# Kernel optimization log

Hardware: AMD Instinct MI355X
Metric: run time of the kernel (lower is better)

Reference implementation:

```python
import jax, jax.numpy as jnp
import numpy as np

BIAS_VALUE = -1e30


def apply_rope(inputs, positions, max_wavelength=10000):
    # inputs: [B, T, H, Dh]; positions: [B, T]
    head_dim = inputs.shape[-1]
    fraction = 2 * jnp.arange(0, head_dim // 2) / head_dim
    timescale = max_wavelength ** fraction
    sinusoid_inp = positions[..., jnp.newaxis] / timescale[jnp.newaxis, :]  # [B, T, Dh/2]
    sinusoid_inp = sinusoid_inp[..., jnp.newaxis, :]                        # [B, T, 1, Dh/2]
    sin = jnp.sin(sinusoid_inp)
    cos = jnp.cos(sinusoid_inp)
    first_half, second_half = jnp.split(inputs, 2, axis=-1)
    first_part = first_half * cos - second_half * sin
    second_part = second_half * cos + first_half * sin
    return jnp.concatenate([first_part, second_part], axis=-1).astype(inputs.dtype)


def rms_norm(x, scale):
    var = jnp.mean(jnp.square(x), axis=-1, keepdims=True)
    return x * jax.lax.rsqrt(var + 1e-6) * (1 + scale)


def setup_inputs() -> dict:
    key = jax.random.key(0)
    ks = jax.random.split(key, 12)
    B, T, D, H, Dh = 4, 2048, 512, 8, 64
    q = jax.random.normal(ks[0], (B, T, D), jnp.float32)
    kv = jax.random.normal(ks[1], (B, T, D), jnp.float32)
    mask = jnp.broadcast_to(jnp.tril(jnp.ones((T, T), bool))[None, None], (B, 1, T, T))
    pos = jnp.broadcast_to(jnp.arange(T, dtype=jnp.int32), (B, T))
    s = 0.02
    return {
        "q": q, "kv": kv, "mask": mask, "q_positions": pos, "kv_positions": pos,
        "wq": jax.random.normal(ks[2], (D, H * Dh), jnp.float32) * s,
        "bq": jnp.zeros((H * Dh,), jnp.float32),
        "wk": jax.random.normal(ks[3], (D, H * Dh), jnp.float32) * s,
        "bk": jnp.zeros((H * Dh,), jnp.float32),
        "wv": jax.random.normal(ks[4], (D, H * Dh), jnp.float32) * s,
        "bv": jnp.zeros((H * Dh,), jnp.float32),
        "scale_q": jax.random.normal(ks[5], (Dh,), jnp.float32) * s,
        "scale_k": jax.random.normal(ks[6], (Dh,), jnp.float32) * s,
        "wo": jax.random.normal(ks[7], (H * Dh, D), jnp.float32) * s,
        "bo": jnp.zeros((D,), jnp.float32),
    }


def reference(q, kv, mask, q_positions, kv_positions,
              wq, bq, wk, bk, wv, bv, scale_q, scale_k, wo, bo):
    B, T, D = q.shape
    H = 8
    Dh = wq.shape[1] // H
    qk_size = Dh

    def proj(x, w, b):
        y = x @ w + b
        return y.reshape(*x.shape[:-1], H, -1)  # [B, T, H, Dh]

    query_heads = rms_norm(proj(q, wq, bq), scale_q)
    key_heads = rms_norm(proj(kv, wk, bk), scale_k)
    value_heads = proj(kv, wv, bv)

    query_heads = apply_rope(query_heads, q_positions)
    key_heads = apply_rope(key_heads, kv_positions)

    attn_logits = jnp.einsum('bthd,bThd->bhtT', query_heads, key_heads)
    attn_logits = attn_logits / np.sqrt(qk_size).astype(q.dtype)
    attn_logits = jnp.where(mask, attn_logits, BIAS_VALUE)
    attn_weights = jax.nn.softmax(attn_logits, axis=-1)
    attn_weights = jnp.where(mask, attn_weights, 0)
    attn = jnp.einsum('bhtT,bThd->bthd', attn_weights, value_heads)
    attn = attn.reshape(B, T, -1)
    return attn @ wo + bo
```

## Files before the change

### kernel.cpp

```cpp
#include <hip/hip_runtime.h>
#include <hip/hip_bf16.h>
#include <cstdint>

#define B_ 4
#define T_ 2048
#define D_ 512
#define H_ 8

typedef __bf16 bf16x8 __attribute__((ext_vector_type(8)));
typedef __bf16 bf16x4 __attribute__((ext_vector_type(4)));
typedef float f32x4 __attribute__((ext_vector_type(4)));

#define QSCALE 0.18033688011112042f
#define MSHIFT 16.0f

__device__ inline void gload_lds16(const void* g, void* l) {
    __builtin_amdgcn_global_load_lds(
        (const __attribute__((address_space(1))) void*)g,
        (__attribute__((address_space(3))) void*)l, 16, 0, 0);
}

__global__ void transpose_w4_kernel(const float* __restrict__ wq, const float* __restrict__ wk,
                                    const float* __restrict__ wv, const float* __restrict__ wo,
                                    __bf16* __restrict__ wqkvT, __bf16* __restrict__ woT) {
    __shared__ float tile[32][33];
    int z = blockIdx.z;
    const float* in = (z == 0) ? wq : (z == 1) ? wk : (z == 2) ? wv : wo;
    __bf16* out = (z < 3) ? wqkvT + (size_t)z * D_ * D_ : woT;
    int tx = threadIdx.x & 31, ty = threadIdx.x >> 5;
    int r0 = blockIdx.y * 32, c0 = blockIdx.x * 32;
#pragma unroll
    for (int i = 0; i < 4; i++)
        tile[ty + i * 8][tx] = in[(size_t)(r0 + ty + i * 8) * D_ + c0 + tx];
    __syncthreads();
#pragma unroll
    for (int i = 0; i < 4; i++)
        out[(size_t)(c0 + ty + i * 8) * D_ + r0 + tx] = (__bf16)tile[tx][ty + i * 8];
}

__global__ void rope_table_kernel(float2* __restrict__ tab) {
    int i = blockIdx.x * 256 + threadIdx.x;
    int p = i >> 5, d2 = i & 31;
    float inv_ts = exp2f((float)d2 * (-13.28771237954945f / 32.0f));
    float ang = (float)p * inv_ts;
    float sv, cv;
    __sincosf(ang, &sv, &cv);
    tab[i] = make_float2(cv, sv);
}

template<int MODE>
__global__ __launch_bounds__(256, 2) void gemm_tile_kernel(
    const float* __restrict__ Aq32, const float* __restrict__ Akv32,
    const __bf16* __restrict__ Xbf,
    const __bf16* __restrict__ WT,
    const float* __restrict__ biasQ, const float* __restrict__ biasK,
    const float* __restrict__ biasV,
    float* __restrict__ outf, __bf16* __restrict__ qh, __bf16* __restrict__ kh,
    __bf16* __restrict__ vt,
    const float* __restrict__ scale_q, const float* __restrict__ scale_k,
    const int* __restrict__ qpos, const int* __restrict__ kpos,
    const float2* __restrict__ rtab, int M, int Ntot, int K) {
    __shared__ __bf16 Ab[2][128 * 32];
    __shared__ __bf16 Bb[2][128 * 32];

    const int tid = threadIdx.x;
    const int lane = tid & 63, widx = tid >> 6;
    const int lo = lane & 15, hi = lane >> 4;
    const int wm = widx >> 1, wn = widx & 1;

    const int nwg = gridDim.x;
    const int q8 = nwg >> 3;
    int bid = blockIdx.x;
    int swz = (bid & 7) * q8 + (bid >> 3);
    const int ntn = Ntot >> 7;
    const int m0 = (swz / ntn) << 7;
    const int nt = swz % ntn;
    const int n0g = nt << 7;
    const int seg = (MODE == 3) ? (nt >> 2) : 0;

    const int srow = tid >> 2;
    const int sslot = tid & 3;

    const float* Af32 = (MODE == 3) ? ((seg > 0) ? Akv32 : Aq32) : nullptr;

    f32x4 acc[4][4] = {};

    auto stageB = [&](int kc, int bufi) {
#pragma unroll
        for (int i = 0; i < 2; i++) {
            int row = i * 64 + srow;
            int cs = sslot ^ ((row >> 1) & 3);
            gload_lds16(WT + (size_t)(n0g + row) * K + kc + cs * 8,
                        &Bb[bufi][(i * 64 + widx * 16) * 32]);
        }
    };
    auto stageA_bf = [&](int kc, int bufi) {
#pragma unroll
        for (int i = 0; i < 2; i++) {
            int row = i * 64 + srow;
            int cs = sslot ^ ((row >> 1) & 3);
            gload_lds16(Xbf + (size_t)(m0 + row) * K + kc + cs * 8,
                        &Ab[bufi][(i * 64 + widx * 16) * 32]);
        }
    };
    auto loadA32 = [&](float4 (&r)[2][2], int kc) {
#pragma unroll
        for (int i = 0; i < 2; i++) {
            const float* src = Af32 + (size_t)(m0 + i * 64 + srow) * K + kc + sslot * 8;
            r[i][0] = *reinterpret_cast<const float4*>(src);
            r[i][1] = *reinterpret_cast<const float4*>(src + 4);
        }
    };
    auto writeA32 = [&](float4 (&r)[2][2], int bufi) {
#pragma unroll
        for (int i = 0; i < 2; i++) {
            int row = i * 64 + srow;
            bf16x8 v = { (__bf16)r[i][0].x, (__bf16)r[i][0].y,
                         (__bf16)r[i][0].z, (__bf16)r[i][0].w,
                         (__bf16)r[i][1].x, (__bf16)r[i][1].y,
                         (__bf16)r[i][1].z, (__bf16)r[i][1].w };
            *reinterpret_cast<bf16x8*>(
                &Ab[bufi][row * 32 + ((sslot ^ ((row >> 1) & 3)) << 3)]) = v;
        }
    };
    auto compute = [&](int bufi) {
        bf16x8 a[4], bvec[4];
#pragma unroll
        for (int mf = 0; mf < 4; mf++) {
            int R = wm * 64 + mf * 16 + lo;
            a[mf] = *reinterpret_cast<const bf16x8*>(&Ab[bufi][R * 32 + ((hi ^ ((R >> 1) & 3)) << 3)]);
        }
#pragma unroll
        for (int nf = 0; nf < 4; nf++) {
            int R = wn * 64 + nf * 16 + lo;
            bvec[nf] = *reinterpret_cast<const bf16x8*>(&Bb[bufi][R * 32 + ((hi ^ ((R >> 1) & 3)) << 3)]);
        }
#pragma unroll
        for (int mf = 0; mf < 4; mf++)
#pragma unroll
            for (int nf = 0; nf < 4; nf++)
                acc[mf][nf] = __builtin_amdgcn_mfma_f32_16x16x32_bf16(a[mf], bvec[nf], acc[mf][nf], 0, 0, 0);
    };

    const int nks = K >> 5;
    int cur = 0;

    if constexpr (MODE == 3) {
        float4 rA[2][2], rB[2][2];
        auto step3 = [&](int ks, float4 (&rUse)[2][2], float4 (&rLoad)[2][2]) {
            if (ks + 2 < nks) loadA32(rLoad, (ks + 2) << 5);
            if (ks + 1 < nks) stageB((ks + 1) << 5, cur ^ 1);
            compute(cur);
            if (ks + 1 < nks) writeA32(rUse, cur ^ 1);
            __syncthreads();
            cur ^= 1;
        };
        loadA32(rA, 0);
        stageB(0, 0);
        writeA32(rA, 0);
        loadA32(rA, 32);
        __syncthreads();
        for (int ks = 0; ks < nks; ks += 2) {
            step3(ks, rA, rB);
            step3(ks + 1, rB, rA);
        }
    } else {
        stageA_bf(0, 0); stageB(0, 0);
        __syncthreads();
        for (int ks = 0; ks < nks; ks++) {
            const int kc2 = (ks + 1) << 5;
            if (ks + 1 < nks) { stageA_bf(kc2, cur ^ 1); stageB(kc2, cur ^ 1); }
            compute(cur);
            __syncthreads();
            cur ^= 1;
        }
    }

    const int mrow0 = m0 + wm * 64;

    if (MODE == 0) {
        const int ncol0 = n0g + wn * 64;
        float bs[4];
#pragma unroll
        for (int nf = 0; nf < 4; nf++) bs[nf] = biasQ[ncol0 + nf * 16 + lo];
#pragma unroll
        for (int mf = 0; mf < 4; mf++)
#pragma unroll
            for (int nf = 0; nf < 4; nf++)
#pragma unroll
                for (int r = 0; r < 4; r++) {
                    int row = mrow0 + mf * 16 + hi * 4 + r;
                    outf[(size_t)row * Ntot + ncol0 + nf * 16 + lo] = acc[mf][nf][r] + bs[nf];
                }
    } else {
        const int ncol0 = ((nt & 3) << 7) + wn * 64;
        const int h = ncol0 >> 6;
        const float* bias = (seg == 0) ? biasQ : (seg == 1) ? biasK : biasV;
        float bs[4];
#pragma unroll
        for (int nf = 0; nf < 4; nf++) bs[nf] = bias[ncol0 + nf * 16 + lo];

        if (seg < 2) {
            const float* scale = seg ? scale_k : scale_q;
            const int* pos = seg ? kpos : qpos;
            __bf16* dst0 = seg ? kh : qh;
            const float qmul = seg ? 1.0f : QSCALE;
            float sc4[4];
#pragma unroll
            for (int nf = 0; nf < 4; nf++) sc4[nf] = (1.0f + scale[nf * 16 + lo]) * qmul;
#pragma unroll
            for (int mf = 0; mf < 4; mf++) {
#pragma unroll
                for (int r = 0; r < 4; r++) {
                    int row = mrow0 + mf * 16 + hi * 4 + r;
                    float y0 = acc[mf][0][r] + bs[0];
                    float y1 = acc[mf][1][r] + bs[1];
                    float y2 = acc[mf][2][r] + bs[2];
                    float y3 = acc[mf][3][r] + bs[3];
                    float ps = y0 * y0 + y1 * y1 + y2 * y2 + y3 * y3;
#pragma unroll
                    for (int off = 1; off < 16; off <<= 1) ps += __shfl_xor(ps, off);
                    float rmsf = rsqrtf(ps * (1.0f / 64.0f) + 1e-6f);
                    int p = pos[row];
                    float2 c0 = rtab[p * 32 + lo];
                    float2 c1 = rtab[p * 32 + 16 + lo];
                    float z0 = y0 * rmsf * sc4[0];
                    float z1 = y1 * rmsf * sc4[1];
                    float z2 = y2 * rmsf * sc4[2];
                    float z3 = y3 * rmsf * sc4[3];
                    int b = row >> 11, t = row & (T_ - 1);
                    __bf16* dst = dst0 + ((size_t)(b * H_ + h) * T_ + t) * 64;
                    dst[lo]      = (__bf16)(z0 * c0.x - z2 * c0.y);
                    dst[16 + lo] = (__bf16)(z1 * c1.x - z3 * c1.y);
                    dst[32 + lo] = (__bf16)(z2 * c0.x + z0 * c0.y);
                    dst[48 + lo] = (__bf16)(z3 * c1.x + z1 * c1.y);
                }
            }
        } else {
#pragma unroll
            for (int mf = 0; mf < 4; mf++) {
                int row0 = mrow0 + mf * 16 + hi * 4;
                int b = row0 >> 11, t0 = row0 & (T_ - 1);
#pragma unroll
                for (int nf = 0; nf < 4; nf++) {
                    int d = nf * 16 + lo;
                    bf16x4 pk = { (__bf16)(acc[mf][nf][0] + bs[nf]), (__bf16)(acc[mf][nf][1] + bs[nf]),
                                  (__bf16)(acc[mf][nf][2] + bs[nf]), (__bf16)(acc[mf][nf][3] + bs[nf]) };
                    *reinterpret_cast<bf16x4*>(vt + ((size_t)(b * H_ + h) * 64 + d) * T_ + t0) = pk;
                }
            }
        }
    }
}

__global__ __launch_bounds__(256, 4) void attn_kernel(const __bf16* __restrict__ qh,
                                                      const __bf16* __restrict__ kh,
                                                      const __bf16* __restrict__ vt,
                                                      __bf16* __restrict__ attn) {
    __shared__ __bf16 kbuf[2][64 * 64];
    __shared__ __bf16 vbuf[2][64 * 64];
    __shared__ __bf16 plds[4][16][64];

    const int lane = threadIdx.x & 63, widx = threadIdx.x >> 6;
    const int lo = lane & 15, hi = lane >> 4;
    const int bh = blockIdx.x;
    const int sid = 31 - blockIdx.y;
    const int ntiles = sid + 1;
    const int qb = sid * 64 + widx * 16;
    const __bf16* Qg = qh + (size_t)bh * T_ * 64;
    const __bf16* Kg = kh + (size_t)bh * T_ * 64;
    const __bf16* Vg = vt + (size_t)bh * 64 * T_;
    const int b = bh >> 3, h = bh & 7;

    const int srow = lane >> 3;
    const int sslot = lane & 7;
    const int schunk = sslot ^ srow;

    bf16x8 qa[2];
#pragma unroll
    for (int c = 0; c < 2; c++)
        qa[c] = *reinterpret_cast<const bf16x8*>(Qg + (size_t)(qb + lo) * 64 + c * 32 + hi * 8);

    f32x4 o[4] = {};
    float l = 0.0f;
    const f32x4 minit = { -MSHIFT, -MSHIFT, -MSHIFT, -MSHIFT };

    auto stage = [&](int tile, int bufi) {
        const int kvb0 = tile * 64;
#pragma unroll
        for (int i = 0; i < 2; i++) {
            int r = widx * 16 + i * 8 + srow;
            gload_lds16(Kg + (size_t)(kvb0 + r) * 64 + schunk * 8,
                        &kbuf[bufi][(widx * 16 + i * 8) * 64]);
        }
#pragma unroll
        for (int i = 0; i < 2; i++) {
            int r = widx * 16 + i * 8 + srow;
            gload_lds16(Vg + (size_t)r * T_ + kvb0 + schunk * 8,
                        &vbuf[bufi][(widx * 16 + i * 8) * 64]);
        }
    };

    stage(0, 0);
    __syncthreads();
    int cur = 0;

    for (int j = 0; j < ntiles; ++j) {
        if (j + 1 < ntiles) stage(j + 1, cur ^ 1);

        f32x4 s[4] = { minit, minit, minit, minit };
        __builtin_amdgcn_s_setprio(1);
#pragma unroll
        for (int c = 0; c < 2; c++) {
#pragma unroll
            for (int f = 0; f < 4; f++) {
                int R = f * 16 + lo;
                int C = c * 4 + hi;
                bf16x8 kb = *reinterpret_cast<const bf16x8*>(
                    &kbuf[cur][R * 64 + ((C ^ (lo & 7)) << 3)]);
                s[f] = __builtin_amdgcn_mfma_f32_16x16x32_bf16(kb, qa[c], s[f], 0, 0, 0);
            }
        }
        __builtin_amdgcn_s_setprio(0);

        if (j == ntiles - 1) {
#pragma unroll
            for (int f = 0; f < 4; f++)
#pragma unroll
                for (int r = 0; r < 4; r++)
                    if (f * 16 + hi * 4 + r > widx * 16 + lo) s[f][r] = -1e30f;
        }

        float ps = 0.0f;
        bf16x4 pk[4];
#pragma unroll
        for (int f = 0; f < 4; f++) {
#pragma unroll
            for (int r = 0; r < 4; r++) {
                float e = __builtin_amdgcn_exp2f(s[f][r]);
                ps += e;
                pk[f][r] = (__bf16)e;
            }
        }
        ps += __shfl_xor(ps, 16);
        ps += __shfl_xor(ps, 32);
        l += ps;

#pragma unroll
        for (int f = 0; f < 4; f++)
            *reinterpret_cast<bf16x4*>(
                &plds[widx][lo][(((f * 2 + (hi >> 1)) ^ (lo & 7)) << 3) + ((hi & 1) << 2)]) = pk[f];
        bf16x8 pa0 = *reinterpret_cast<const bf16x8*>(&plds[widx][lo][((hi) ^ (lo & 7)) << 3]);
        bf16x8 pa1 = *reinterpret_cast<const bf16x8*>(&plds[widx][lo][((4 + hi) ^ (lo & 7)) << 3]);

        __builtin_amdgcn_s_setprio(1);
#pragma unroll
        for (int n = 0; n < 4; n++) {
#pragma unroll
            for (int c = 0; c < 2; c++) {
                int R = n * 16 + lo;
                int C = c * 4 + hi;
                bf16x8 vb = *reinterpret_cast<const bf16x8*>(
                    &vbuf[cur][R * 64 + ((C ^ (lo & 7)) << 3)]);
                o[n] = __builtin_amdgcn_mfma_f32_16x16x32_bf16(vb, c ? pa1 : pa0, o[n], 0, 0, 0);
            }
        }
        __builtin_amdgcn_s_setprio(0);

        __syncthreads();
        cur ^= 1;
    }

    const float inv = 1.0f / l;
    const int qrow = qb + lo;
#pragma unroll
    for (int n = 0; n < 4; n++) {
        bf16x4 pko = { (__bf16)(o[n][0] * inv), (__bf16)(o[n][1] * inv),
                       (__bf16)(o[n][2] * inv), (__bf16)(o[n][3] * inv) };
        *reinterpret_cast<bf16x4*>(attn + ((size_t)b * T_ + qrow) * D_ + h * 64 + n * 16 + hi * 4) = pko;
    }
}

extern "C" void kernel_launch(void* const* d_in, const int* in_sizes, int n_in,
                              void* d_out, int out_size, void* d_ws, size_t ws_size,
                              hipStream_t stream) {
    const float* q  = (const float*)d_in[0];
    const float* kv = (const float*)d_in[1];
    const int* qpos = (const int*)d_in[3];
    const int* kpos = (const int*)d_in[4];
    const float* wq = (const float*)d_in[5];
    const float* bq = (const float*)d_in[6];
    const float* wk = (const float*)d_in[7];
    const float* bk = (const float*)d_in[8];
    const float* wv = (const float*)d_in[9];
    const float* bv = (const float*)d_in[10];
    const float* scale_q = (const float*)d_in[11];
    const float* scale_k = (const float*)d_in[12];
    const float* wo = (const float*)d_in[13];
    const float* bo = (const float*)d_in[14];
    float* out = (float*)d_out;

    char* ws = (char*)d_ws;
    size_t off = 0;
    auto alloc = [&](size_t bytes) {
        void* p = ws + off;
        off += (bytes + 255) & ~(size_t)255;
        return p;
    };
    const size_t MD = (size_t)B_ * T_ * D_;
    __bf16* wqkvT  = (__bf16*)alloc((size_t)3 * D_ * D_ * 2);
    __bf16* woT    = (__bf16*)alloc((size_t)D_ * D_ * 2);
    __bf16* qh    = (__bf16*)alloc(MD * 2);
    __bf16* kh    = (__bf16*)alloc(MD * 2);
    __bf16* vt    = (__bf16*)alloc(MD * 2);
    __bf16* attnb = (__bf16*)alloc(MD * 2);
    float2* rtab = (float2*)alloc((size_t)T_ * 32 * sizeof(float2));

    transpose_w4_kernel<<<dim3(16, 16, 4), 256, 0, stream>>>(wq, wk, wv, wo, wqkvT, woT);
    rope_table_kernel<<<(T_ * 32) / 256, 256, 0, stream>>>(rtab);

    const int M = B_ * T_;
    gemm_tile_kernel<3><<<(M / 128) * (3 * D_ / 128), 256, 0, stream>>>(
        q, kv, nullptr, wqkvT, bq, bk, bv, nullptr, qh, kh, vt,
        scale_q, scale_k, qpos, kpos, rtab, M, 3 * D_, D_);
    attn_kernel<<<dim3(B_ * H_, 32), 256, 0, stream>>>(qh, kh, vt, attnb);
    gemm_tile_kernel<0><<<(M / 128) * (D_ / 128), 256, 0, stream>>>(
        nullptr, nullptr, attnb, woT, bo, nullptr, nullptr, out, nullptr, nullptr, nullptr,
        nullptr, nullptr, nullptr, nullptr, nullptr, M, D_, D_);
}
```

Before: 84.51 us.

## Split long causal attention strips across two blocks and merge partial outputs

Query strips with sid >= 16 are split into two KV ranges handled by separate blocks, using a lookup table that orders work units so that loads stay balanced. Each half writes its unnormalized fp32 output and row sum to a workspace, and a new merge kernel adds the halves and normalizes. The aim is to shorten the critical path set by the longest causal strips and balance load across CUs. The cost is an extra kernel launch plus fp32 partial-output traffic. Since the softmax uses a fixed max shift and no running max, the partial results can simply be added.

Measured after the change: 91.60 us. +8.4%, slower.

```diff
diff --git a/kernel.cpp b/kernel.cpp
--- a/kernel.cpp
+++ b/kernel.cpp
@@ -253,19 +253,39 @@
     }
 }
 
+static __device__ const uint8_t UNIT_SID[48] = {
+    31,31,30,15, 30,29,29,28,14, 28,27,27,26,13, 26,25,25,24,12,
+    24,23,23,22,11, 22,21,21,20,10, 20,19,19,18,9, 18,17,17,16,8,
+    16,7, 6,5,4,3,2,1,0 };
+static __device__ const uint8_t UNIT_T0[48] = {
+    0,16,0,0, 16,0,15,0,0, 15,0,14,0,0, 14,0,13,0,0,
+    13,0,12,0,0, 12,0,11,0,0, 11,0,10,0,0, 10,0,9,0,0,
+    9,0, 0,0,0,0,0,0,0 };
+static __device__ const uint8_t UNIT_T1[48] = {
+    16,32,16,16, 31,15,30,15,15, 29,14,28,14,14, 27,13,26,13,13,
+    25,12,24,12,12, 23,11,22,11,11, 21,10,20,10,10, 19,9,18,9,9,
+    17,8, 7,6,5,4,3,2,1 };
+
 __global__ __launch_bounds__(256, 4) void attn_kernel(const __bf16* __restrict__ qh,
                                                       const __bf16* __restrict__ kh,
                                                       const __bf16* __restrict__ vt,
-                                                      __bf16* __restrict__ attn) {
+                                                      __bf16* __restrict__ attn,
+                                                      float* __restrict__ O_ws,
+                                                      float* __restrict__ l_ws) {
     __shared__ __bf16 kbuf[2][64 * 64];
     __shared__ __bf16 vbuf[2][64 * 64];
     __shared__ __bf16 plds[4][16][64];
 
     const int lane = threadIdx.x & 63, widx = threadIdx.x >> 6;
     const int lo = lane & 15, hi = lane >> 4;
-    const int bh = blockIdx.x;
-    const int sid = 31 - blockIdx.y;
-    const int ntiles = sid + 1;
+    const int idx = blockIdx.x;
+    const int bh = idx & 31;
+    const int u = idx >> 5;
+    const int sid = UNIT_SID[u];
+    const int t0 = UNIT_T0[u];
+    const int t1 = UNIT_T1[u];
+    const bool split = (sid >= 16);
+    const int part = (t0 != 0) ? 1 : 0;
     const int qb = sid * 64 + widx * 16;
     const __bf16* Qg = qh + (size_t)bh * T_ * 64;
     const __bf16* Kg = kh + (size_t)bh * T_ * 64;
@@ -301,12 +321,12 @@
         }
     };
 
-    stage(0, 0);
+    stage(t0, 0);
     __syncthreads();
     int cur = 0;
 
-    for (int j = 0; j < ntiles; ++j) {
-        if (j + 1 < ntiles) stage(j + 1, cur ^ 1);
+    for (int j = t0; j < t1; ++j) {
+        if (j + 1 < t1) stage(j + 1, cur ^ 1);
 
         f32x4 s[4] = { minit, minit, minit, minit };
         __builtin_amdgcn_s_setprio(1);
@@ -323,7 +343,7 @@
         }
         __builtin_amdgcn_s_setprio(0);
 
-        if (j == ntiles - 1) {
+        if (j == sid) {
 #pragma unroll
             for (int f = 0; f < 4; f++)
 #pragma unroll
@@ -371,13 +391,47 @@
         cur ^= 1;
     }
 
-    const float inv = 1.0f / l;
-    const int qrow = qb + lo;
-#pragma unroll
-    for (int n = 0; n < 4; n++) {
-        bf16x4 pko = { (__bf16)(o[n][0] * inv), (__bf16)(o[n][1] * inv),
-                       (__bf16)(o[n][2] * inv), (__bf16)(o[n][3] * inv) };
-        *reinterpret_cast<bf16x4*>(attn + ((size_t)b * T_ + qrow) * D_ + h * 64 + n * 16 + hi * 4) = pko;
+    if (!split) {
+        const float inv = 1.0f / l;
+        const int qrow = qb + lo;
+#pragma unroll
+        for (int n = 0; n < 4; n++) {
+            bf16x4 pko = { (__bf16)(o[n][0] * inv), (__bf16)(o[n][1] * inv),
+                           (__bf16)(o[n][2] * inv), (__bf16)(o[n][3] * inv) };
+            *reinterpret_cast<bf16x4*>(attn + ((size_t)b * T_ + qrow) * D_ + h * 64 + n * 16 + hi * 4) = pko;
+        }
+    } else {
+        const int qrl = widx * 16 + lo;
+        const size_t slot = ((size_t)bh * 16 + (sid - 16)) * 2 + part;
+        float* Obase = O_ws + (slot * 64 + qrl) * 64;
+#pragma unroll
+        for (int n = 0; n < 4; n++)
+            *reinterpret_cast<f32x4*>(Obase + n * 16 + hi * 4) = o[n];
+        if (hi == 0) l_ws[slot * 64 + qrl] = l;
+    }
+}
+
+__global__ void attn_merge_kernel(const float* __restrict__ O_ws, const float* __restrict__ l_ws,
+                                  __bf16* __restrict__ attn) {
+    const int blk = blockIdx.x;
+    const int bh = blk & 31, s16 = blk >> 5;
+    const int sid = 16 + s16;
+    const int t = threadIdx.x;
+    const int row = t >> 2, cq = (t & 3) << 4;
+    const size_t base = ((size_t)bh * 16 + s16) * 2;
+    const float* O0 = O_ws + ((base + 0) * 64 + row) * 64 + cq;
+    const float* O1 = O_ws + ((base + 1) * 64 + row) * 64 + cq;
+    const float inv = 1.0f / (l_ws[(base + 0) * 64 + row] + l_ws[(base + 1) * 64 + row]);
+    const int b = bh >> 3, h = bh & 7;
+    const int q = sid * 64 + row;
+    __bf16* dst = attn + ((size_t)b * T_ + q) * D_ + h * 64 + cq;
+#pragma unroll
+    for (int c = 0; c < 16; c += 4) {
+        f32x4 a = *reinterpret_cast<const f32x4*>(O0 + c);
+        f32x4 bb = *reinterpret_cast<const f32x4*>(O1 + c);
+        bf16x4 ov = { (__bf16)((a[0] + bb[0]) * inv), (__bf16)((a[1] + bb[1]) * inv),
+                      (__bf16)((a[2] + bb[2]) * inv), (__bf16)((a[3] + bb[3]) * inv) };
+        *reinterpret_cast<bf16x4*>(dst + c) = ov;
     }
 }
 
@@ -415,6 +469,8 @@
     __bf16* vt    = (__bf16*)alloc(MD * 2);
     __bf16* attnb = (__bf16*)alloc(MD * 2);
     float2* rtab = (float2*)alloc((size_t)T_ * 32 * sizeof(float2));
+    float* O_ws = (float*)alloc((size_t)32 * 16 * 2 * 64 * 64 * 4);
+    float* l_ws = (float*)alloc((size_t)32 * 16 * 2 * 64 * 4);
 
     transpose_w4_kernel<<<dim3(16, 16, 4), 256, 0, stream>>>(wq, wk, wv, wo, wqkvT, woT);
     rope_table_kernel<<<(T_ * 32) / 256, 256, 0, stream>>>(rtab);
@@ -423,7 +479,8 @@
     gemm_tile_kernel<3><<<(M / 128) * (3 * D_ / 128), 256, 0, stream>>>(
         q, kv, nullptr, wqkvT, bq, bk, bv, nullptr, qh, kh, vt,
         scale_q, scale_k, qpos, kpos, rtab, M, 3 * D_, D_);
-    attn_kernel<<<dim3(B_ * H_, 32), 256, 0, stream>>>(qh, kh, vt, attnb);
+    attn_kernel<<<1536, 256, 0, stream>>>(qh, kh, vt, attnb, O_ws, l_ws);
+    attn_merge_kernel<<<512, 256, 0, stream>>>(O_ws, l_ws, attnb);
     gemm_tile_kernel<0><<<(M / 128) * (D_ / 128), 256, 0, stream>>>(
         nullptr, nullptr, attnb, woT, bo, nullptr, nullptr, out, nullptr, nullptr, nullptr,
         nullptr, nullptr, nullptr, nullptr, nullptr, M, D_, D_);
```

## Restructure attention into independent 32-row waves reading K/V directly from global

Applied to the files above, without the earlier changes.

Rewrites the attention kernel so each wave owns 32 query rows and independently loops over key tiles, loading K and V fragments straight from global memory rather than staging them through shared memory with barriers. Pairs a short and a long causal row block in one 128-thread workgroup to balance work, and launches 1024 blocks. This removes LDS staging and __syncthreads cost but depends on the cache for K/V reuse across waves, and exposes global load latency with no explicit prefetch.

Result: slower. 128.8 us (+52.4%).

```diff
diff --git a/kernel.cpp b/kernel.cpp
--- a/kernel.cpp
+++ b/kernel.cpp
@@ -253,131 +253,118 @@
     }
 }
 
-__global__ __launch_bounds__(256, 4) void attn_kernel(const __bf16* __restrict__ qh,
+__global__ __launch_bounds__(128, 2) void attn_kernel(const __bf16* __restrict__ qh,
                                                       const __bf16* __restrict__ kh,
                                                       const __bf16* __restrict__ vt,
                                                       __bf16* __restrict__ attn) {
-    __shared__ __bf16 kbuf[2][64 * 64];
-    __shared__ __bf16 vbuf[2][64 * 64];
-    __shared__ __bf16 plds[4][16][64];
+    __shared__ __bf16 plds[2][32][64];
 
     const int lane = threadIdx.x & 63, widx = threadIdx.x >> 6;
     const int lo = lane & 15, hi = lane >> 4;
-    const int bh = blockIdx.x;
-    const int sid = 31 - blockIdx.y;
-    const int ntiles = sid + 1;
-    const int qb = sid * 64 + widx * 16;
+    const int bh = blockIdx.x & 31;
+    const int pairIdx = blockIdx.x >> 5;
+    const int p = widx ? (63 - pairIdx) : pairIdx;
+    const int qb = p * 32;
+    const int jmax = p >> 1;
     const __bf16* Qg = qh + (size_t)bh * T_ * 64;
     const __bf16* Kg = kh + (size_t)bh * T_ * 64;
     const __bf16* Vg = vt + (size_t)bh * 64 * T_;
     const int b = bh >> 3, h = bh & 7;
 
-    const int srow = lane >> 3;
-    const int sslot = lane & 7;
-    const int schunk = sslot ^ srow;
-
-    bf16x8 qa[2];
-#pragma unroll
-    for (int c = 0; c < 2; c++)
-        qa[c] = *reinterpret_cast<const bf16x8*>(Qg + (size_t)(qb + lo) * 64 + c * 32 + hi * 8);
-
-    f32x4 o[4] = {};
-    float l = 0.0f;
+    bf16x8 qa[2][2];
+#pragma unroll
+    for (int g = 0; g < 2; g++)
+#pragma unroll
+        for (int c = 0; c < 2; c++)
+            qa[g][c] = *reinterpret_cast<const bf16x8*>(
+                Qg + (size_t)(qb + g * 16 + lo) * 64 + c * 32 + hi * 8);
+
+    f32x4 o[2][4] = {};
+    float l[2] = { 0.0f, 0.0f };
     const f32x4 minit = { -MSHIFT, -MSHIFT, -MSHIFT, -MSHIFT };
 
-    auto stage = [&](int tile, int bufi) {
-        const int kvb0 = tile * 64;
-#pragma unroll
-        for (int i = 0; i < 2; i++) {
-            int r = widx * 16 + i * 8 + srow;
-            gload_lds16(Kg + (size_t)(kvb0 + r) * 64 + schunk * 8,
-                        &kbuf[bufi][(widx * 16 + i * 8) * 64]);
-        }
-#pragma unroll
-        for (int i = 0; i < 2; i++) {
-            int r = widx * 16 + i * 8 + srow;
-            gload_lds16(Vg + (size_t)r * T_ + kvb0 + schunk * 8,
-                        &vbuf[bufi][(widx * 16 + i * 8) * 64]);
-        }
-    };
-
-    stage(0, 0);
-    __syncthreads();
-    int cur = 0;
-
-    for (int j = 0; j < ntiles; ++j) {
-        if (j + 1 < ntiles) stage(j + 1, cur ^ 1);
-
-        f32x4 s[4] = { minit, minit, minit, minit };
+    for (int j = 0; j <= jmax; ++j) {
+        const int kvb = j * 64;
+
+        f32x4 s[2][4] = { { minit, minit, minit, minit }, { minit, minit, minit, minit } };
         __builtin_amdgcn_s_setprio(1);
 #pragma unroll
         for (int c = 0; c < 2; c++) {
 #pragma unroll
             for (int f = 0; f < 4; f++) {
-                int R = f * 16 + lo;
-                int C = c * 4 + hi;
                 bf16x8 kb = *reinterpret_cast<const bf16x8*>(
-                    &kbuf[cur][R * 64 + ((C ^ (lo & 7)) << 3)]);
-                s[f] = __builtin_amdgcn_mfma_f32_16x16x32_bf16(kb, qa[c], s[f], 0, 0, 0);
+                    Kg + (size_t)(kvb + f * 16 + lo) * 64 + c * 32 + hi * 8);
+                s[0][f] = __builtin_amdgcn_mfma_f32_16x16x32_bf16(kb, qa[0][c], s[0][f], 0, 0, 0);
+                s[1][f] = __builtin_amdgcn_mfma_f32_16x16x32_bf16(kb, qa[1][c], s[1][f], 0, 0, 0);
             }
         }
         __builtin_amdgcn_s_setprio(0);
 
-        if (j == ntiles - 1) {
+        if (j == jmax) {
+#pragma unroll
+            for (int g = 0; g < 2; g++)
+#pragma unroll
+                for (int f = 0; f < 4; f++)
+#pragma unroll
+                    for (int r = 0; r < 4; r++)
+                        if (kvb + f * 16 + hi * 4 + r > qb + g * 16 + lo) s[g][f][r] = -1e30f;
+        }
+
+        bf16x4 pk[2][4];
+#pragma unroll
+        for (int g = 0; g < 2; g++) {
+            float ps = 0.0f;
 #pragma unroll
             for (int f = 0; f < 4; f++)
 #pragma unroll
-                for (int r = 0; r < 4; r++)
-                    if (f * 16 + hi * 4 + r > widx * 16 + lo) s[f][r] = -1e30f;
-        }
-
-        float ps = 0.0f;
-        bf16x4 pk[4];
-#pragma unroll
-        for (int f = 0; f < 4; f++) {
-#pragma unroll
-            for (int r = 0; r < 4; r++) {
-                float e = __builtin_amdgcn_exp2f(s[f][r]);
-                ps += e;
-                pk[f][r] = (__bf16)e;
+                for (int r = 0; r < 4; r++) {
+                    float e = __builtin_amdgcn_exp2f(s[g][f][r]);
+                    ps += e;
+                    pk[g][f][r] = (__bf16)e;
+                }
+            ps += __shfl_xor(ps, 16);
+            ps += __shfl_xor(ps, 32);
+            l[g] += ps;
+        }
+
+#pragma unroll
+        for (int g = 0; g < 2; g++)
+#pragma unroll
+            for (int f = 0; f < 4; f++)
+                *reinterpret_cast<bf16x4*>(
+                    &plds[widx][g * 16 + lo][(((f * 2 + (hi >> 1)) ^ (lo & 7)) << 3) + ((hi & 1) << 2)]) = pk[g][f];
+        bf16x8 pa[2][2];
+#pragma unroll
+        for (int g = 0; g < 2; g++)
+#pragma unroll
+            for (int c = 0; c < 2; c++)
+                pa[g][c] = *reinterpret_cast<const bf16x8*>(
+                    &plds[widx][g * 16 + lo][((c * 4 + hi) ^ (lo & 7)) << 3]);
+
+        __builtin_amdgcn_s_setprio(1);
+#pragma unroll
+        for (int n = 0; n < 4; n++) {
+#pragma unroll
+            for (int c = 0; c < 2; c++) {
+                bf16x8 vb = *reinterpret_cast<const bf16x8*>(
+                    Vg + (size_t)(n * 16 + lo) * T_ + kvb + c * 32 + hi * 8);
+                o[0][n] = __builtin_amdgcn_mfma_f32_16x16x32_bf16(vb, pa[0][c], o[0][n], 0, 0, 0);
+                o[1][n] = __builtin_amdgcn_mfma_f32_16x16x32_bf16(vb, pa[1][c], o[1][n], 0, 0, 0);
             }
         }
-        ps += __shfl_xor(ps, 16);
-        ps += __shfl_xor(ps, 32);
-        l += ps;
-
-#pragma unroll
-        for (int f = 0; f < 4; f++)
-            *reinterpret_cast<bf16x4*>(
-                &plds[widx][lo][(((f * 2 + (hi >> 1)) ^ (lo & 7)) << 3) + ((hi & 1) << 2)]) = pk[f];
-        bf16x8 pa0 = *reinterpret_cast<const bf16x8*>(&plds[widx][lo][((hi) ^ (lo & 7)) << 3]);
-        bf16x8 pa1 = *reinterpret_cast<const bf16x8*>(&plds[widx][lo][((4 + hi) ^ (lo & 7)) << 3]);
-
-        __builtin_amdgcn_s_setprio(1);
+        __builtin_amdgcn_s_setprio(0);
+    }
+
+#pragma unroll
+    for (int g = 0; g < 2; g++) {
+        const float inv = 1.0f / l[g];
+        const int qrow = qb + g * 16 + lo;
 #pragma unroll
         for (int n = 0; n < 4; n++) {
-#pragma unroll
-            for (int c = 0; c < 2; c++) {
-                int R = n * 16 + lo;
-                int C = c * 4 + hi;
-                bf16x8 vb = *reinterpret_cast<const bf16x8*>(
-                    &vbuf[cur][R * 64 + ((C ^ (lo & 7)) << 3)]);
-                o[n] = __builtin_amdgcn_mfma_f32_16x16x32_bf16(vb, c ? pa1 : pa0, o[n], 0, 0, 0);
-            }
-        }
-        __builtin_amdgcn_s_setprio(0);
-
-        __syncthreads();
-        cur ^= 1;
-    }
-
-    const float inv = 1.0f / l;
-    const int qrow = qb + lo;
-#pragma unroll
-    for (int n = 0; n < 4; n++) {
-        bf16x4 pko = { (__bf16)(o[n][0] * inv), (__bf16)(o[n][1] * inv),
-                       (__bf16)(o[n][2] * inv), (__bf16)(o[n][3] * inv) };
-        *reinterpret_cast<bf16x4*>(attn + ((size_t)b * T_ + qrow) * D_ + h * 64 + n * 16 + hi * 4) = pko;
+            bf16x4 pko = { (__bf16)(o[g][n][0] * inv), (__bf16)(o[g][n][1] * inv),
+                           (__bf16)(o[g][n][2] * inv), (__bf16)(o[g][n][3] * inv) };
+            *reinterpret_cast<bf16x4*>(attn + ((size_t)b * T_ + qrow) * D_ + h * 64 + n * 16 + hi * 4) = pko;
+        }
     }
 }
 
@@ -423,7 +410,7 @@
     gemm_tile_kernel<3><<<(M / 128) * (3 * D_ / 128), 256, 0, stream>>>(
         q, kv, nullptr, wqkvT, bq, bk, bv, nullptr, qh, kh, vt,
         scale_q, scale_k, qpos, kpos, rtab, M, 3 * D_, D_);
-    attn_kernel<<<dim3(B_ * H_, 32), 256, 0, stream>>>(qh, kh, vt, attnb);
+    attn_kernel<<<1024, 128, 0, stream>>>(qh, kh, vt, attnb);
     gemm_tile_kernel<0><<<(M / 128) * (D_ / 128), 256, 0, stream>>>(
         nullptr, nullptr, attnb, woT, bo, nullptr, nullptr, out, nullptr, nullptr, nullptr,
         nullptr, nullptr, nullptr, nullptr, nullptr, M, D_, D_);
```
